# Kernel tuning notes

Hardware: AMD Instinct MI355X
Metric: run time of the kernel (lower is better)

Reference implementation:

```python
import jax, jax.numpy as jnp
import numpy as np

N_FILTER, S_SUB, D_IN, K_STEP, TAO = 8, 5, 64, 3, 0.05
B, N = 100000, 100000


def setup_inputs() -> dict:
    key = jax.random.key(0)
    k1, k2, k3, k4, k5 = jax.random.split(key, 5)
    adjs = jax.random.uniform(k1, (B, S_SUB, S_SUB), jnp.float32)
    feature = jax.random.normal(k2, (N, D_IN), jnp.float32)
    idxs = jax.random.randint(k3, (B, S_SUB), 0, N)  # indexes into feature; row N is the zero pad row
    adjs_hidden = jax.random.uniform(k4, (N_FILTER, S_SUB * (S_SUB - 1) // 2), jnp.float32, minval=-1.0, maxval=1.0)
    features_hidden = jax.random.uniform(k5, (N_FILTER, S_SUB, D_IN), jnp.float32, minval=-1.0, maxval=1.0)
    return dict(adjs=adjs, feature=feature, idxs=idxs, adjs_hidden=adjs_hidden, features_hidden=features_hidden)


def _greedy_mask(total):
    # total: [B, F, m, s]. Greedy row-by-row argmax matching, columns consumed once.
    B_, F_, m, s = total.shape
    taken0 = jnp.zeros((B_, F_, s), bool).at[:, :, 0].set(True)  # column 0 reserved for row 0

    def step(taken, row_scores):  # row_scores: [B, F, s]
        scores = jnp.where(taken, jnp.asarray(-1.0, total.dtype), row_scores)
        idx = jnp.argmax(scores, axis=-1)  # [B, F]
        oh = jax.nn.one_hot(idx, s, dtype=total.dtype)
        return jnp.logical_or(taken, oh > 0), oh

    xs = jnp.moveaxis(total[:, :, 1:, :], 2, 0)  # [m-1, B, F, s]
    _, rows = jax.lax.scan(step, taken0, xs)  # rows: [m-1, B, F, s]
    row0 = jnp.zeros((B_, F_, s), total.dtype).at[:, :, 0].set(1.0)
    mask = jnp.concatenate([row0[None], rows], axis=0)  # [m, B, F, s]
    return jnp.moveaxis(mask, 0, 2)  # [B, F, m, s]


def reference(adjs, feature, idxs, adjs_hidden, features_hidden):
    F_, s, d = features_hidden.shape
    # symmetric hidden adjacency from sigmoid of upper-triangular params
    sig = jax.nn.sigmoid(adjs_hidden)
    iu0, iu1 = np.triu_indices(s, 1)
    A_h = (jnp.zeros((F_, s, s), adjs_hidden.dtype)
           .at[:, iu0, iu1].set(sig)
           .at[:, iu1, iu0].set(sig))
    # pad features with a zero row, gather subgraph node features
    feat = jnp.concatenate([feature, jnp.zeros((1, feature.shape[1]), feature.dtype)], axis=0)
    f = feat[idxs]  # [B, m, d]
    fh = features_hidden  # [F, s, d]

    total = jnp.zeros((f.shape[0], F_, f.shape[1], s), f.dtype)
    for hop in range(K_STEP):
        if hop != 0:
            f = jnp.einsum('bij,bjd->bid', adjs, f)
            fh = jnp.einsum('fij,fjd->fid', A_h, fh)
        sq_f = jnp.sum(f * f, axis=-1)    # [B, m]
        sq_h = jnp.sum(fh * fh, axis=-1)  # [F, s]
        cross = jnp.einsum('bme,fse->bfms', f, fh)  # [B, F, m, s]
        dist = sq_f[:, None, :, None] + sq_h[None, :, None, :] - 2.0 * cross
        total = total + jnp.exp(-dist / d / TAO)

    mask = _greedy_mask(total)
    return jnp.sum(total * mask, axis=(2, 3))  # [B, F]
```

## Files before the change

### kernel.cpp

```cpp
#include <hip/hip_runtime.h>
#include <math.h>

#define NF 8
#define SS 5
#define DIN 64
#define KSTEP 3
#define BT 32
#define FH_PAD 68
#define FSTR (SS*FH_PAD)
#define HOPSTR (NF*FSTR)
#define NS_OFF (KSTEP*HOPSTR)

#define CS 0.45084219902780109f
#define CC 0.90168439805560218f

__device__ __forceinline__ float fexp2(float x) {
#if __has_builtin(__builtin_amdgcn_exp2f)
  return __builtin_amdgcn_exp2f(x);
#else
  return exp2f(x);
#endif
}

__global__ __launch_bounds__(256) void hidden_prep(
    const float* __restrict__ adjs_hidden,
    const float* __restrict__ features_hidden,
    float* __restrict__ ws)
{
  __shared__ float Ah[NF][SS][SS];
  __shared__ float buf[2][NF][SS][DIN];
  const int t = threadIdx.x;

  if (t < NF*SS*SS) ((float*)Ah)[t] = 0.0f;
  for (int i = t; i < NF*SS*DIN; i += 256) ((float*)buf[0])[i] = features_hidden[i];
  __syncthreads();
  if (t < NF*10) {
    const int iu0[10] = {0,0,0,0,1,1,1,2,2,3};
    const int iu1[10] = {1,2,3,4,2,3,4,3,4,4};
    int f = t / 10, k = t % 10;
    float sg = 1.0f / (1.0f + expf(-adjs_hidden[t]));
    Ah[f][iu0[k]][iu1[k]] = sg;
    Ah[f][iu1[k]][iu0[k]] = sg;
  }
  __syncthreads();

  int cur = 0;
  for (int h = 0; h < KSTEP; ++h) {
    for (int i = t; i < NF*SS*DIN; i += 256) {
      int f = i / (SS*DIN), s = (i / DIN) % SS, d = i % DIN;
      ws[h*HOPSTR + f*FSTR + s*FH_PAD + d] = buf[cur][f][s][d];
    }
    if (t < NF*SS) {
      float acc = 0.0f;
      int f = t / SS, s = t % SS;
      for (int d = 0; d < DIN; ++d) { float v = buf[cur][f][s][d]; acc = fmaf(v, v, acc); }
      ws[NS_OFF + h*NF*SS + t] = -acc * CS;
    }
    if (h + 1 < KSTEP) {
      __syncthreads();
      for (int i = t; i < NF*SS*DIN; i += 256) {
        int f = i / (SS*DIN), s = (i / DIN) % SS, d = i % DIN;
        float acc = 0.0f;
        for (int j = 0; j < SS; ++j) acc = fmaf(Ah[f][s][j], buf[cur][f][j][d], acc);
        buf[cur^1][f][s][d] = acc;
      }
      __syncthreads();
      cur ^= 1;
    }
  }
}

__global__ __launch_bounds__(256) void kc_main(
    const float* __restrict__ adjs,
    const float* __restrict__ feature,
    const int* __restrict__ idxs,
    const float* __restrict__ ws,
    float* __restrict__ out,
    int B, int N)
{
  __shared__ float fh[KSTEP*HOPSTR];
  __shared__ float nsqh[KSTEP*NF*SS];
  __shared__ float fS[BT][SS][FH_PAD];

  const int t    = threadIdx.x;
  const int lane = t & 63;
  const int wv   = t >> 6;
  const int b_i  = t >> 3;
  const int f_   = t & 7;
  const int bg   = blockIdx.x * BT + b_i;
  const bool valid = bg < B;

  for (int c = wv; c < 32; c += 4) {
    const int nfl = (c == 31) ? 224 : 256;
    if (lane * 4 < nfl)
      __builtin_amdgcn_global_load_lds(
          (const __attribute__((address_space(1))) void*)(ws + c*256 + lane*4),
          (__attribute__((address_space(3))) void*)(fh + c*256), 16, 0, 0);
  }
  if (t < KSTEP*NF*SS) nsqh[t] = ws[NS_OFF + t];

  float a[SS*SS];
  #pragma unroll
  for (int k = 0; k < SS*SS; ++k)
    a[k] = valid ? adjs[(size_t)bg*(SS*SS) + k] : 0.0f;

  #pragma unroll
  for (int m = 0; m < SS; ++m) {
    int id = valid ? idxs[bg*SS + m] : -1;
    #pragma unroll
    for (int h2 = 0; h2 < 2; ++h2) {
      float4 v = make_float4(0.f, 0.f, 0.f, 0.f);
      if ((unsigned)id < (unsigned)N)
        v = reinterpret_cast<const float4*>(feature)[(size_t)id*16 + f_*2 + h2];
      *reinterpret_cast<float4*>(&fS[b_i][m][f_*8 + h2*4]) = v;
    }
  }

  __syncthreads();

  float total[SS][SS];
  #pragma unroll
  for (int m = 0; m < SS; ++m)
    #pragma unroll
    for (int s = 0; s < SS; ++s) total[m][s] = 0.0f;

  #pragma unroll 1
  for (int hop = 0; hop < KSTEP; ++hop) {
    if (hop) {
      const int dbase = f_ * 8;
      float fo[SS][8];
      #pragma unroll
      for (int j = 0; j < SS; ++j)
        #pragma unroll
        for (int h2 = 0; h2 < 2; ++h2) {
          float4 v = *reinterpret_cast<const float4*>(&fS[b_i][j][dbase + h2*4]);
          fo[j][h2*4+0] = v.x; fo[j][h2*4+1] = v.y;
          fo[j][h2*4+2] = v.z; fo[j][h2*4+3] = v.w;
        }
      #pragma unroll
      for (int m = 0; m < SS; ++m) {
        float fn[8];
        #pragma unroll
        for (int dd = 0; dd < 8; ++dd) fn[dd] = 0.0f;
        #pragma unroll
        for (int j = 0; j < SS; ++j)
          #pragma unroll
          for (int dd = 0; dd < 8; ++dd)
            fn[dd] = fmaf(a[m*SS + j], fo[j][dd], fn[dd]);
        #pragma unroll
        for (int h2 = 0; h2 < 2; ++h2) {
          float4 v = make_float4(fn[h2*4+0], fn[h2*4+1], fn[h2*4+2], fn[h2*4+3]);
          *reinterpret_cast<float4*>(&fS[b_i][m][dbase + h2*4]) = v;
        }
      }
    }

    float cr[SS][SS], sqf[SS];
    #pragma unroll
    for (int m = 0; m < SS; ++m) {
      sqf[m] = 0.0f;
      #pragma unroll
      for (int s = 0; s < SS; ++s) cr[m][s] = 0.0f;
    }

    const float* fhh = &fh[hop*HOPSTR + f_*FSTR];
    #pragma unroll
    for (int d4 = 0; d4 < 16; ++d4) {
      float4 fv[SS], hv[SS];
      #pragma unroll
      for (int m = 0; m < SS; ++m)
        fv[m] = *reinterpret_cast<const float4*>(&fS[b_i][m][d4*4]);
      #pragma unroll
      for (int s = 0; s < SS; ++s)
        hv[s] = *reinterpret_cast<const float4*>(&fhh[s*FH_PAD + d4*4]);
      #pragma unroll
      for (int m = 0; m < SS; ++m) {
        sqf[m] = fmaf(fv[m].x, fv[m].x, sqf[m]);
        sqf[m] = fmaf(fv[m].y, fv[m].y, sqf[m]);
        sqf[m] = fmaf(fv[m].z, fv[m].z, sqf[m]);
        sqf[m] = fmaf(fv[m].w, fv[m].w, sqf[m]);
        #pragma unroll
        for (int s = 0; s < SS; ++s) {
          cr[m][s] = fmaf(fv[m].x, hv[s].x, cr[m][s]);
          cr[m][s] = fmaf(fv[m].y, hv[s].y, cr[m][s]);
          cr[m][s] = fmaf(fv[m].z, hv[s].z, cr[m][s]);
          cr[m][s] = fmaf(fv[m].w, hv[s].w, cr[m][s]);
        }
      }
    }

    #pragma unroll
    for (int m = 0; m < SS; ++m) {
      float sm = sqf[m] * CS;
      #pragma unroll
      for (int s = 0; s < SS; ++s) {
        float nh = nsqh[hop*NF*SS + f_*SS + s];
        float arg = fmaf(CC, cr[m][s], nh - sm);
        total[m][s] += fexp2(arg);
      }
    }
  }

  float res = total[0][0];
  int taken = 1;
  #pragma unroll
  for (int r = 1; r < SS; ++r) {
    float best = -2.0f; int bi = 0;
    #pragma unroll
    for (int s = 0; s < SS; ++s) {
      float sc = ((taken >> s) & 1) ? -1.0f : total[r][s];
      if (sc > best) { best = sc; bi = s; }
    }
    res += best;
    taken |= (1 << bi);
  }
  if (valid) out[(size_t)bg*NF + f_] = res;
}

extern "C" void kernel_launch(void* const* d_in, const int* in_sizes, int n_in,
                              void* d_out, int out_size, void* d_ws, size_t ws_size,
                              hipStream_t stream) {
  const float* adjs            = (const float*)d_in[0];
  const float* feature         = (const float*)d_in[1];
  const int*   idxs            = (const int*)d_in[2];
  const float* adjs_hidden     = (const float*)d_in[3];
  const float* features_hidden = (const float*)d_in[4];
  float* out = (float*)d_out;
  float* ws  = (float*)d_ws;

  const int B = in_sizes[0] / (SS*SS);
  const int N = in_sizes[1] / DIN;

  hipLaunchKernelGGL(hidden_prep, dim3(1), dim3(256), 0, stream,
                     adjs_hidden, features_hidden, ws);
  const int nblk = (B + BT - 1) / BT;
  hipLaunchKernelGGL(kc_main, dim3(nblk), dim3(256), 0, stream,
                     adjs, feature, idxs, ws, out, B, N);
}
```

Measured before the change: 134.3 us.

## Replace per-hop feature propagation with small-matrix recurrences on cross and Gram terms

Instead of propagating 64-dim subgraph features through adjs and recomputing dot products each hop, the kernel computes the hop-0 cross matrix and a 5x5 Gram matrix once. Later hops update them algebraically: C <- A C Ah^T and M <- A M A^T. This removes two hops of 64-wide FMA work and LDS traffic per (b,f) thread, and shrinks the shared hidden-feature tile to hop 0 only. In exchange it adds small 5x5 matrix products per thread, an extra LDS exchange for the Gram entries, and may change floating-point rounding.

```diff
diff --git a/kernel.cpp b/kernel.cpp
--- a/kernel.cpp
+++ b/kernel.cpp
@@ -8,8 +8,9 @@
 #define BT 32
 #define FH_PAD 68
 #define FSTR (SS*FH_PAD)
-#define HOPSTR (NF*FSTR)
-#define NS_OFF (KSTEP*HOPSTR)
+#define FH0_SZ (NF*FSTR)
+#define NSQ_OFF FH0_SZ
+#define AH_OFF  (FH0_SZ + KSTEP*NF*SS)
 
 #define CS 0.45084219902780109f
 #define CC 0.90168439805560218f
@@ -20,6 +21,16 @@
 #else
   return exp2f(x);
 #endif
+}
+
+__device__ __forceinline__ constexpr int midx(int i, int j) {
+  return (i <= j) ? (i*(9-i))/2 + j : (j*(9-j))/2 + i;
+}
+
+__device__ __forceinline__ void tri_ij(int e, int& i, int& j) {
+  int i_ = (e >= 5) + (e >= 9) + (e >= 12) + (e >= 14);
+  int off = (i_ == 0) ? 0 : (i_ == 1) ? 4 : (i_ == 2) ? 7 : (i_ == 3) ? 9 : 10;
+  i = i_; j = e - off;
 }
 
 __global__ __launch_bounds__(256) void hidden_prep(
@@ -44,17 +55,21 @@
   }
   __syncthreads();
 
+  if (t < NF*SS*SS) ws[AH_OFF + t] = ((float*)Ah)[t];
+
   int cur = 0;
   for (int h = 0; h < KSTEP; ++h) {
-    for (int i = t; i < NF*SS*DIN; i += 256) {
-      int f = i / (SS*DIN), s = (i / DIN) % SS, d = i % DIN;
-      ws[h*HOPSTR + f*FSTR + s*FH_PAD + d] = buf[cur][f][s][d];
+    if (h == 0) {
+      for (int i = t; i < NF*SS*DIN; i += 256) {
+        int f = i / (SS*DIN), s = (i / DIN) % SS, d = i % DIN;
+        ws[f*FSTR + s*FH_PAD + d] = buf[cur][f][s][d];
+      }
     }
     if (t < NF*SS) {
       float acc = 0.0f;
       int f = t / SS, s = t % SS;
       for (int d = 0; d < DIN; ++d) { float v = buf[cur][f][s][d]; acc = fmaf(v, v, acc); }
-      ws[NS_OFF + h*NF*SS + t] = -acc * CS;
+      ws[NSQ_OFF + h*NF*SS + t] = -acc * CS;
     }
     if (h + 1 < KSTEP) {
       __syncthreads();
@@ -78,9 +93,10 @@
     float* __restrict__ out,
     int B, int N)
 {
-  __shared__ float fh[KSTEP*HOPSTR];
+  __shared__ float fh[FH0_SZ];
   __shared__ float nsqh[KSTEP*NF*SS];
   __shared__ float fS[BT][SS][FH_PAD];
+  __shared__ float Msh[BT][17];
 
   const int t    = threadIdx.x;
   const int lane = t & 63;
@@ -90,19 +106,18 @@
   const int bg   = blockIdx.x * BT + b_i;
   const bool valid = bg < B;
 
-  for (int c = wv; c < 32; c += 4) {
-    const int nfl = (c == 31) ? 224 : 256;
-    if (lane * 4 < nfl)
+  for (int c = wv; c < 11; c += 4) {
+    if (c < 10 || lane < 40)
       __builtin_amdgcn_global_load_lds(
           (const __attribute__((address_space(1))) void*)(ws + c*256 + lane*4),
           (__attribute__((address_space(3))) void*)(fh + c*256), 16, 0, 0);
   }
-  if (t < KSTEP*NF*SS) nsqh[t] = ws[NS_OFF + t];
-
-  float a[SS*SS];
+  if (t < KSTEP*NF*SS) nsqh[t] = ws[NSQ_OFF + t];
+
+  float A_[SS*SS];
   #pragma unroll
   for (int k = 0; k < SS*SS; ++k)
-    a[k] = valid ? adjs[(size_t)bg*(SS*SS) + k] : 0.0f;
+    A_[k] = valid ? adjs[(size_t)bg*(SS*SS) + k] : 0.0f;
 
   #pragma unroll
   for (int m = 0; m < SS; ++m) {
@@ -118,87 +133,146 @@
 
   __syncthreads();
 
+  float C[SS][SS];
+  #pragma unroll
+  for (int m = 0; m < SS; ++m)
+    #pragma unroll
+    for (int s = 0; s < SS; ++s) C[m][s] = 0.0f;
+
+  const float* fhh = &fh[f_*FSTR];
+  #pragma unroll
+  for (int d4 = 0; d4 < 16; ++d4) {
+    float4 fv[SS], hv[SS];
+    #pragma unroll
+    for (int m = 0; m < SS; ++m)
+      fv[m] = *reinterpret_cast<const float4*>(&fS[b_i][m][d4*4]);
+    #pragma unroll
+    for (int s = 0; s < SS; ++s)
+      hv[s] = *reinterpret_cast<const float4*>(&fhh[s*FH_PAD + d4*4]);
+    #pragma unroll
+    for (int m = 0; m < SS; ++m)
+      #pragma unroll
+      for (int s = 0; s < SS; ++s) {
+        C[m][s] = fmaf(fv[m].x, hv[s].x, C[m][s]);
+        C[m][s] = fmaf(fv[m].y, hv[s].y, C[m][s]);
+        C[m][s] = fmaf(fv[m].z, hv[s].z, C[m][s]);
+        C[m][s] = fmaf(fv[m].w, hv[s].w, C[m][s]);
+      }
+  }
+
+  int i0, j0, i1, j1;
+  tri_ij(f_, i0, j0);
+  const int e1 = f_ + 8;
+  tri_ij(e1 > 14 ? 14 : e1, i1, j1);
+  {
+    const float* fb = &fS[b_i][0][0];
+    const float* r0 = fb + i0*FH_PAD;
+    const float* r1 = fb + j0*FH_PAD;
+    const float* r2 = fb + i1*FH_PAD;
+    const float* r3 = fb + j1*FH_PAD;
+    float m0 = 0.0f, m1 = 0.0f;
+    #pragma unroll
+    for (int d4 = 0; d4 < 16; ++d4) {
+      float4 va = *reinterpret_cast<const float4*>(&r0[d4*4]);
+      float4 vb = *reinterpret_cast<const float4*>(&r1[d4*4]);
+      float4 vc = *reinterpret_cast<const float4*>(&r2[d4*4]);
+      float4 vd = *reinterpret_cast<const float4*>(&r3[d4*4]);
+      m0 = fmaf(va.x, vb.x, m0); m0 = fmaf(va.y, vb.y, m0);
+      m0 = fmaf(va.z, vb.z, m0); m0 = fmaf(va.w, vb.w, m0);
+      m1 = fmaf(vc.x, vd.x, m1); m1 = fmaf(vc.y, vd.y, m1);
+      m1 = fmaf(vc.z, vd.z, m1); m1 = fmaf(vc.w, vd.w, m1);
+    }
+    Msh[b_i][f_] = m0;
+    if (e1 < 15) Msh[b_i][e1] = m1;
+  }
+  float M[15];
+  #pragma unroll
+  for (int e = 0; e < 15; ++e) M[e] = Msh[b_i][e];
+
   float total[SS][SS];
-  #pragma unroll
-  for (int m = 0; m < SS; ++m)
-    #pragma unroll
-    for (int s = 0; s < SS; ++s) total[m][s] = 0.0f;
-
-  #pragma unroll 1
-  for (int hop = 0; hop < KSTEP; ++hop) {
-    if (hop) {
-      const int dbase = f_ * 8;
-      float fo[SS][8];
-      #pragma unroll
-      for (int j = 0; j < SS; ++j)
-        #pragma unroll
-        for (int h2 = 0; h2 < 2; ++h2) {
-          float4 v = *reinterpret_cast<const float4*>(&fS[b_i][j][dbase + h2*4]);
-          fo[j][h2*4+0] = v.x; fo[j][h2*4+1] = v.y;
-          fo[j][h2*4+2] = v.z; fo[j][h2*4+3] = v.w;
+
+  {
+    float nh[SS];
+    #pragma unroll
+    for (int s = 0; s < SS; ++s) nh[s] = nsqh[0*NF*SS + f_*SS + s];
+    #pragma unroll
+    for (int m = 0; m < SS; ++m) {
+      float sm = CS * M[midx(m, m)];
+      #pragma unroll
+      for (int s = 0; s < SS; ++s)
+        total[m][s] = fexp2(fmaf(CC, C[m][s], nh[s] - sm));
+    }
+  }
+
+  float Ah_[SS*SS];
+  #pragma unroll
+  for (int k = 0; k < SS*SS; ++k)
+    Ah_[k] = ws[AH_OFF + f_*SS*SS + k];
+
+  #pragma unroll
+  for (int hop = 1; hop < KSTEP; ++hop) {
+    float T[SS][SS];
+    #pragma unroll
+    for (int i = 0; i < SS; ++i)
+      #pragma unroll
+      for (int k = 0; k < SS; ++k) {
+        float acc = 0.0f;
+        #pragma unroll
+        for (int j = 0; j < SS; ++j) acc = fmaf(A_[i*SS+j], C[j][k], acc);
+        T[i][k] = acc;
+      }
+    #pragma unroll
+    for (int i = 0; i < SS; ++i)
+      #pragma unroll
+      for (int s = 0; s < SS; ++s) {
+        float acc = 0.0f;
+        #pragma unroll
+        for (int k = 0; k < SS; ++k) acc = fmaf(T[i][k], Ah_[s*SS+k], acc);
+        C[i][s] = acc;
+      }
+
+    float TM[SS][SS];
+    #pragma unroll
+    for (int i = 0; i < SS; ++i)
+      #pragma unroll
+      for (int l = 0; l < SS; ++l) {
+        float acc = 0.0f;
+        #pragma unroll
+        for (int k = 0; k < SS; ++k) acc = fmaf(A_[i*SS+k], M[midx(k, l)], acc);
+        TM[i][l] = acc;
+      }
+
+    float sqf2[SS];
+    if (hop + 1 < KSTEP) {
+      #pragma unroll
+      for (int i = 0; i < SS; ++i)
+        #pragma unroll
+        for (int j = i; j < SS; ++j) {
+          float acc = 0.0f;
+          #pragma unroll
+          for (int l = 0; l < SS; ++l) acc = fmaf(TM[i][l], A_[j*SS+l], acc);
+          M[midx(i, j)] = acc;
         }
       #pragma unroll
+      for (int m = 0; m < SS; ++m) sqf2[m] = CS * M[midx(m, m)];
+    } else {
+      #pragma unroll
       for (int m = 0; m < SS; ++m) {
-        float fn[8];
-        #pragma unroll
-        for (int dd = 0; dd < 8; ++dd) fn[dd] = 0.0f;
-        #pragma unroll
-        for (int j = 0; j < SS; ++j)
-          #pragma unroll
-          for (int dd = 0; dd < 8; ++dd)
-            fn[dd] = fmaf(a[m*SS + j], fo[j][dd], fn[dd]);
-        #pragma unroll
-        for (int h2 = 0; h2 < 2; ++h2) {
-          float4 v = make_float4(fn[h2*4+0], fn[h2*4+1], fn[h2*4+2], fn[h2*4+3]);
-          *reinterpret_cast<float4*>(&fS[b_i][m][dbase + h2*4]) = v;
-        }
-      }
-    }
-
-    float cr[SS][SS], sqf[SS];
-    #pragma unroll
-    for (int m = 0; m < SS; ++m) {
-      sqf[m] = 0.0f;
-      #pragma unroll
-      for (int s = 0; s < SS; ++s) cr[m][s] = 0.0f;
-    }
-
-    const float* fhh = &fh[hop*HOPSTR + f_*FSTR];
-    #pragma unroll
-    for (int d4 = 0; d4 < 16; ++d4) {
-      float4 fv[SS], hv[SS];
-      #pragma unroll
-      for (int m = 0; m < SS; ++m)
-        fv[m] = *reinterpret_cast<const float4*>(&fS[b_i][m][d4*4]);
+        float acc = 0.0f;
+        #pragma unroll
+        for (int l = 0; l < SS; ++l) acc = fmaf(TM[m][l], A_[m*SS+l], acc);
+        sqf2[m] = CS * acc;
+      }
+    }
+
+    float nh[SS];
+    #pragma unroll
+    for (int s = 0; s < SS; ++s) nh[s] = nsqh[hop*NF*SS + f_*SS + s];
+    #pragma unroll
+    for (int m = 0; m < SS; ++m)
       #pragma unroll
       for (int s = 0; s < SS; ++s)
-        hv[s] = *reinterpret_cast<const float4*>(&fhh[s*FH_PAD + d4*4]);
-      #pragma unroll
-      for (int m = 0; m < SS; ++m) {
-        sqf[m] = fmaf(fv[m].x, fv[m].x, sqf[m]);
-        sqf[m] = fmaf(fv[m].y, fv[m].y, sqf[m]);
-        sqf[m] = fmaf(fv[m].z, fv[m].z, sqf[m]);
-        sqf[m] = fmaf(fv[m].w, fv[m].w, sqf[m]);
-        #pragma unroll
-        for (int s = 0; s < SS; ++s) {
-          cr[m][s] = fmaf(fv[m].x, hv[s].x, cr[m][s]);
-          cr[m][s] = fmaf(fv[m].y, hv[s].y, cr[m][s]);
-          cr[m][s] = fmaf(fv[m].z, hv[s].z, cr[m][s]);
-          cr[m][s] = fmaf(fv[m].w, hv[s].w, cr[m][s]);
-        }
-      }
-    }
-
-    #pragma unroll
-    for (int m = 0; m < SS; ++m) {
-      float sm = sqf[m] * CS;
-      #pragma unroll
-      for (int s = 0; s < SS; ++s) {
-        float nh = nsqh[hop*NF*SS + f_*SS + s];
-        float arg = fmaf(CC, cr[m][s], nh - sm);
-        total[m][s] += fexp2(arg);
-      }
-    }
+        total[m][s] += fexp2(fmaf(CC, C[m][s], nh[s] - sqf2[m]));
   }
 
   float res = total[0][0];
```

Result: slower. 388.7 us (+189.4%).
